# Performance work log

Measured on AMD Instinct MI355X. Metric: run time of the kernel, lower is better.

The kernel has to match this reference:

```python
import jax, jax.numpy as jnp
import numpy as np

B, IN_DIM, EXP_DIM, E = 16384, 256, 128, 8  # batch, input_dim, expert_dim, expert_num


def setup_inputs() -> dict:
    key = jax.random.key(0)
    ks = jax.random.split(key, 12)
    s_in = 1.0 / np.sqrt(IN_DIM)
    return {
        "x_a": jax.random.normal(ks[0], (B, IN_DIM), jnp.float32),
        "x_b": jax.random.normal(ks[1], (B, IN_DIM), jnp.float32),
        "x_share": jax.random.normal(ks[2], (B, IN_DIM), jnp.float32),
        # expert banks: [E, IN_DIM, EXP_DIM] weights, [E, EXP_DIM] bias
        "Wa": jax.random.uniform(ks[3], (E, IN_DIM, EXP_DIM), jnp.float32, -s_in, s_in),
        "ba": jax.random.uniform(ks[4], (E, EXP_DIM), jnp.float32, -s_in, s_in),
        "Wb": jax.random.uniform(ks[5], (E, IN_DIM, EXP_DIM), jnp.float32, -s_in, s_in),
        "bb": jax.random.uniform(ks[6], (E, EXP_DIM), jnp.float32, -s_in, s_in),
        "Ws": jax.random.uniform(ks[7], (E, IN_DIM, EXP_DIM), jnp.float32, -s_in, s_in),
        "bs": jax.random.uniform(ks[8], (E, EXP_DIM), jnp.float32, -s_in, s_in),
        # gate projections (bias=False): num single-output linears == one [num, IN_DIM] matrix
        "Ga": jax.random.uniform(ks[9], (2 * E, IN_DIM), jnp.float32, -s_in, s_in),
        "Gb": jax.random.uniform(ks[10], (2 * E, IN_DIM), jnp.float32, -s_in, s_in),
        "Gs": jax.random.uniform(ks[11], (3 * E, IN_DIM), jnp.float32, -s_in, s_in),
    }


def _experts(x, W, b):
    # batched dense stack: [B,IN] x [E,IN,D] -> [B,E,D]
    return jnp.einsum("bi,eid->bed", x, W) + b[None, :, :]


def _gate(x, G, experts):
    # logits [B, num]; softmax over experts; weighted sum over expert axis
    w = jax.nn.softmax(x @ G.T, axis=1)
    return jnp.einsum("be,bed->bd", w, experts)


def reference(x_a, x_b, x_share, Wa, ba, Wb, bb, Ws, bs, Ga, Gb, Gs):
    ea = _experts(x_a, Wa, ba)          # [B,E,D]
    eb = _experts(x_b, Wb, bb)          # [B,E,D]
    es = _experts(x_share, Ws, bs)      # [B,E,D]
    out_a = _gate(x_a, Ga, jnp.concatenate([ea, es], axis=1))
    out_b = _gate(x_b, Gb, jnp.concatenate([eb, es], axis=1))
    out_s = _gate(x_share, Gs, jnp.concatenate([ea, eb, es], axis=1))
    return (out_a, out_b, out_s)
```

## Files before the change

### kernel.cpp

```cpp
#include <hip/hip_runtime.h>
#include <stdint.h>

#define BATCH 16384
#define INDIM 256
#define DDIM  128
#define NEXP  8
#define ROWS  32

typedef __bf16 bfv8  __attribute__((ext_vector_type(8)));
typedef float  f32x4 __attribute__((ext_vector_type(4)));

__global__ void prep_kernel(const float* __restrict__ Wa, const float* __restrict__ Wb,
                            const float* __restrict__ Ws, const float* __restrict__ Ga,
                            const float* __restrict__ Gb, const float* __restrict__ Gs,
                            __bf16* __restrict__ wp, __bf16* __restrict__ gp) {
    int t = blockIdx.x * 256 + threadIdx.x;
    const int NW = 3 * 8 * 8 * 8 * 64;
    if (t < NW) {
        int lane = t & 63, nt = (t >> 6) & 7, kt = (t >> 9) & 7, e = (t >> 12) & 7, st = t >> 15;
        const float* W = (st == 0) ? Wa : (st == 1) ? Wb : Ws;
        int d  = nt * 16 + (lane & 15);
        int i0 = kt * 32 + (lane >> 4) * 8;
        __bf16* o = wp + (size_t)t * 8;
#pragma unroll
        for (int j = 0; j < 8; j++)
            o[j] = (__bf16)W[(size_t)(e * 256 + i0 + j) * 128 + d];
    } else if (t < NW + 2048) {
        int t2 = t - NW;
        int lane = t2 & 63, nt = (t2 >> 6) & 3, kt = t2 >> 8;
        int g  = nt * 16 + (lane & 15);
        int k0 = kt * 32 + (lane >> 4) * 8;
        __bf16* o = gp + (size_t)t2 * 8;
#pragma unroll
        for (int j = 0; j < 8; j++) {
            int k = k0 + j;
            float v = 0.f;
            if (g < 16)      v = Ga[g * 256 + k];
            else if (g < 32) v = Gb[(g - 16) * 256 + k];
            else if (g < 56) v = Gs[(g - 32) * 256 + k];
            o[j] = (__bf16)v;
        }
    }
}

__device__ __forceinline__ void load_afr(const float* __restrict__ x, int r0,
                                         int l16, int quad, bfv8 afr[2][8]) {
#pragma unroll
    for (int mt = 0; mt < 2; mt++) {
        const float* xr = x + (size_t)(r0 + mt * 16 + l16) * INDIM;
#pragma unroll
        for (int kt = 0; kt < 8; kt++) {
            f32x4 lo = *(const f32x4*)(xr + kt * 32 + quad * 8);
            f32x4 hi = *(const f32x4*)(xr + kt * 32 + quad * 8 + 4);
            bfv8 a;
            a[0] = (__bf16)lo[0]; a[1] = (__bf16)lo[1]; a[2] = (__bf16)lo[2]; a[3] = (__bf16)lo[3];
            a[4] = (__bf16)hi[0]; a[5] = (__bf16)hi[1]; a[6] = (__bf16)hi[2]; a[7] = (__bf16)hi[3];
            afr[mt][kt] = a;
        }
    }
}

__launch_bounds__(256, 2)
__global__ void ple_kernel(const float* __restrict__ xa, const float* __restrict__ xb,
                           const float* __restrict__ xs,
                           const float* __restrict__ ba, const float* __restrict__ bb,
                           const float* __restrict__ bs,
                           const __bf16* __restrict__ wp, const __bf16* __restrict__ gp,
                           float* __restrict__ out) {
    __shared__ float lgt[ROWS * 64];
    __shared__ float wT[64 * ROWS];

    const int tid  = threadIdx.x;
    const int w    = tid >> 6;
    const int lane = tid & 63;
    const int quad = lane >> 4;
    const int l16  = lane & 15;
    const int r0   = blockIdx.x * ROWS;

    bfv8 afr[2][8];

    {
        const float* x = (w == 0) ? xa : (w == 1) ? xb : xs;
        load_afr(x, r0, l16, quad, afr);
        f32x4 acc[2];
#pragma unroll
        for (int mt = 0; mt < 2; mt++) { f32x4 z = {0.f, 0.f, 0.f, 0.f}; acc[mt] = z; }
#pragma unroll
        for (int kt = 0; kt < 8; kt++) {
            bfv8 g = *(const bfv8*)(gp + ((size_t)(kt * 4 + w) * 64 + lane) * 8);
#pragma unroll
            for (int mt = 0; mt < 2; mt++)
                acc[mt] = __builtin_amdgcn_mfma_f32_16x16x32_bf16(afr[mt][kt], g, acc[mt], 0, 0, 0);
        }
#pragma unroll
        for (int mt = 0; mt < 2; mt++)
#pragma unroll
            for (int r = 0; r < 4; r++)
                lgt[(mt * 16 + quad * 4 + r) * 64 + w * 16 + l16] = acc[mt][r];
    }
    __syncthreads();

    if (tid < ROWS) {
        const float* L = lgt + tid * 64;
#pragma unroll
        for (int gi = 0; gi < 3; gi++) {
            const int base = (gi == 0) ? 0 : (gi == 1 ? 16 : 32);
            const int cnt  = (gi == 2) ? 24 : 16;
            float m = -1e30f;
            for (int k = 0; k < cnt; k++) m = fmaxf(m, L[base + k]);
            float s = 0.f;
            for (int k = 0; k < cnt; k++) s += __expf(L[base + k] - m);
            float inv = 1.f / s;
            for (int k = 0; k < cnt; k++) wT[(base + k) * ROWS + tid] = __expf(L[base + k] - m) * inv;
        }
    }
    __syncthreads();

    float o[3][2][2][4];
#pragma unroll
    for (int oi = 0; oi < 3; oi++)
#pragma unroll
        for (int mt = 0; mt < 2; mt++)
#pragma unroll
            for (int ntl = 0; ntl < 2; ntl++)
#pragma unroll
                for (int r = 0; r < 4; r++) o[oi][mt][ntl][r] = 0.f;

#define FOLD(oi, gbase)                                                            \
    {                                                                              \
        _Pragma("unroll")                                                          \
        for (int mt = 0; mt < 2; mt++) {                                           \
            f32x4 wv = *(const f32x4*)(wT + (gbase + eb) * ROWS + mt * 16 + quad * 4); \
            _Pragma("unroll")                                                      \
            for (int ntl = 0; ntl < 2; ntl++)                                      \
                _Pragma("unroll")                                                  \
                for (int r = 0; r < 4; r++)                                        \
                    o[oi][mt][ntl][r] += wv[r] * acc[mt][ntl][r];                  \
        }                                                                          \
    }

    const __bf16* colb = wp + (size_t)(2 * w) * 512 + (size_t)lane * 8;

    bfv8 cb[4][2];
#pragma unroll
    for (int i = 0; i < 4; i++) {
        cb[i][0] = *(const bfv8*)(colb + (size_t)i * 4096);
        cb[i][1] = *(const bfv8*)(colb + (size_t)i * 4096 + 512);
    }

#pragma unroll
    for (int st = 0; st < 3; st++) {
        const float* x    = (st == 0) ? xa : (st == 1) ? xb : xs;
        const float* bias = (st == 0) ? ba : (st == 1) ? bb : bs;
        load_afr(x, r0, l16, quad, afr);

#pragma unroll 1
        for (int eb = 0; eb < NEXP; eb++) {
            float b0 = bias[eb * 128 + w * 32 + l16];
            float b1 = bias[eb * 128 + w * 32 + 16 + l16];

            f32x4 acc[2][2];
#pragma unroll
            for (int mt = 0; mt < 2; mt++)
#pragma unroll
                for (int ntl = 0; ntl < 2; ntl++) { f32x4 z = {0.f, 0.f, 0.f, 0.f}; acc[mt][ntl] = z; }

#pragma unroll
            for (int kt = 0; kt < 8; kt++) {
                const int sl = kt & 3;
                acc[0][0] = __builtin_amdgcn_mfma_f32_16x16x32_bf16(afr[0][kt], cb[sl][0], acc[0][0], 0, 0, 0);
                acc[1][0] = __builtin_amdgcn_mfma_f32_16x16x32_bf16(afr[1][kt], cb[sl][0], acc[1][0], 0, 0, 0);
                acc[0][1] = __builtin_amdgcn_mfma_f32_16x16x32_bf16(afr[0][kt], cb[sl][1], acc[0][1], 0, 0, 0);
                acc[1][1] = __builtin_amdgcn_mfma_f32_16x16x32_bf16(afr[1][kt], cb[sl][1], acc[1][1], 0, 0, 0);
                if (kt < 4 || st < 2 || eb < NEXP - 1) {
                    size_t gpf = (size_t)(st * 64 + eb * 8 + kt + 4) * 4096;
                    cb[sl][0] = *(const bfv8*)(colb + gpf);
                    cb[sl][1] = *(const bfv8*)(colb + gpf + 512);
                }
            }

#pragma unroll
            for (int mt = 0; mt < 2; mt++)
#pragma unroll
                for (int r = 0; r < 4; r++) { acc[mt][0][r] += b0; acc[mt][1][r] += b1; }

            if (st == 0)      { FOLD(0, 0);  FOLD(2, 32); }
            else if (st == 1) { FOLD(1, 16); FOLD(2, 40); }
            else              { FOLD(0, 8);  FOLD(1, 24); FOLD(2, 48); }
        }
    }
#undef FOLD

#pragma unroll
    for (int oi = 0; oi < 3; oi++) {
        float* ob = out + (size_t)oi * BATCH * DDIM;
#pragma unroll
        for (int mt = 0; mt < 2; mt++)
#pragma unroll
            for (int r = 0; r < 4; r++) {
                int row = r0 + mt * 16 + quad * 4 + r;
#pragma unroll
                for (int ntl = 0; ntl < 2; ntl++)
                    ob[(size_t)row * DDIM + w * 32 + ntl * 16 + l16] = o[oi][mt][ntl][r];
            }
    }
}

extern "C" void kernel_launch(void* const* d_in, const int* in_sizes, int n_in,
                              void* d_out, int out_size, void* d_ws, size_t ws_size,
                              hipStream_t stream) {
    const float* xa = (const float*)d_in[0];
    const float* xb = (const float*)d_in[1];
    const float* xs = (const float*)d_in[2];
    const float* Wa = (const float*)d_in[3];
    const float* ba = (const float*)d_in[4];
    const float* Wb = (const float*)d_in[5];
    const float* bb = (const float*)d_in[6];
    const float* Ws = (const float*)d_in[7];
    const float* bs = (const float*)d_in[8];
    const float* Ga = (const float*)d_in[9];
    const float* Gb = (const float*)d_in[10];
    const float* Gs = (const float*)d_in[11];

    __bf16* wp = (__bf16*)d_ws;
    __bf16* gp = wp + 3 * 8 * 8 * 8 * 64 * 8;

    prep_kernel<<<392, 256, 0, stream>>>(Wa, Wb, Ws, Ga, Gb, Gs, wp, gp);
    ple_kernel<<<BATCH / ROWS, 256, 0, stream>>>(xa, xb, xs, ba, bb, bs, wp, gp, (float*)d_out);
}
```

Measured before the change: 166.6 us.

## Use 512-thread blocks with shared bf16 activations and warp-parallel softmax

Blocks grow to 8 waves, each owning 16 output columns instead of 32. The three input tiles are converted to bf16 once, cooperatively, and staged in shared memory instead of each wave loading and converting them into registers. The gate softmax now runs inside the MFMA waves using shuffle reductions, replacing the serial 32-thread loop. This aims to cut redundant global loads and register pressure so occupancy rises, at the cost of more shared-memory reads in the inner loop and extra barriers.

```diff
diff --git a/kernel.cpp b/kernel.cpp
--- a/kernel.cpp
+++ b/kernel.cpp
@@ -43,32 +43,16 @@
     }
 }
 
-__device__ __forceinline__ void load_afr(const float* __restrict__ x, int r0,
-                                         int l16, int quad, bfv8 afr[2][8]) {
-#pragma unroll
-    for (int mt = 0; mt < 2; mt++) {
-        const float* xr = x + (size_t)(r0 + mt * 16 + l16) * INDIM;
-#pragma unroll
-        for (int kt = 0; kt < 8; kt++) {
-            f32x4 lo = *(const f32x4*)(xr + kt * 32 + quad * 8);
-            f32x4 hi = *(const f32x4*)(xr + kt * 32 + quad * 8 + 4);
-            bfv8 a;
-            a[0] = (__bf16)lo[0]; a[1] = (__bf16)lo[1]; a[2] = (__bf16)lo[2]; a[3] = (__bf16)lo[3];
-            a[4] = (__bf16)hi[0]; a[5] = (__bf16)hi[1]; a[6] = (__bf16)hi[2]; a[7] = (__bf16)hi[3];
-            afr[mt][kt] = a;
-        }
-    }
-}
-
-__launch_bounds__(256, 2)
+__launch_bounds__(512, 4)
 __global__ void ple_kernel(const float* __restrict__ xa, const float* __restrict__ xb,
                            const float* __restrict__ xs,
                            const float* __restrict__ ba, const float* __restrict__ bb,
                            const float* __restrict__ bs,
                            const __bf16* __restrict__ wp, const __bf16* __restrict__ gp,
                            float* __restrict__ out) {
-    __shared__ float lgt[ROWS * 64];
-    __shared__ float wT[64 * ROWS];
+    __shared__ __bf16 xlds[3 * 16 * 512];
+    __shared__ float  wT[64 * ROWS];
+    __shared__ float  pm[2][ROWS], ps[2][ROWS], cm[ROWS], civ[ROWS];
 
     const int tid  = threadIdx.x;
     const int w    = tid >> 6;
@@ -77,112 +61,157 @@
     const int l16  = lane & 15;
     const int r0   = blockIdx.x * ROWS;
 
-    bfv8 afr[2][8];
-
-    {
-        const float* x = (w == 0) ? xa : (w == 1) ? xb : xs;
-        load_afr(x, r0, l16, quad, afr);
-        f32x4 acc[2];
-#pragma unroll
-        for (int mt = 0; mt < 2; mt++) { f32x4 z = {0.f, 0.f, 0.f, 0.f}; acc[mt] = z; }
+    const __bf16* colb = wp + (size_t)w * 512 + (size_t)lane * 8;
+    bfv8 cb[8];
+#pragma unroll
+    for (int i = 0; i < 8; i++)
+        cb[i] = *(const bfv8*)(colb + (size_t)i * 4096);
+
+#pragma unroll
+    for (int i = 0; i < 6; i++) {
+        int gidx = w * 6 + i;
+        int st = gidx >> 4, rem = gidx & 15, mt = rem >> 3, kt = rem & 7;
+        const float* x = (st == 0) ? xa : (st == 1) ? xb : xs;
+        const float* xr = x + (size_t)(r0 + mt * 16 + l16) * INDIM + kt * 32 + quad * 8;
+        f32x4 lo = *(const f32x4*)xr;
+        f32x4 hi = *(const f32x4*)(xr + 4);
+        bfv8 a;
+        a[0] = (__bf16)lo[0]; a[1] = (__bf16)lo[1]; a[2] = (__bf16)lo[2]; a[3] = (__bf16)lo[3];
+        a[4] = (__bf16)hi[0]; a[5] = (__bf16)hi[1]; a[6] = (__bf16)hi[2]; a[7] = (__bf16)hi[3];
+        *(bfv8*)&xlds[(size_t)(st * 16 + mt * 8 + kt) * 512 + lane * 8] = a;
+    }
+    __syncthreads();
+
+    float e_[2][4], mx_[2][4];
+    if (w < 4) {
+        const int gst = (w < 2) ? w : 2;
+        f32x4 acc0 = {0.f, 0.f, 0.f, 0.f}, acc1 = {0.f, 0.f, 0.f, 0.f};
 #pragma unroll
         for (int kt = 0; kt < 8; kt++) {
-            bfv8 g = *(const bfv8*)(gp + ((size_t)(kt * 4 + w) * 64 + lane) * 8);
-#pragma unroll
-            for (int mt = 0; mt < 2; mt++)
-                acc[mt] = __builtin_amdgcn_mfma_f32_16x16x32_bf16(afr[mt][kt], g, acc[mt], 0, 0, 0);
-        }
-#pragma unroll
-        for (int mt = 0; mt < 2; mt++)
+            bfv8 g  = *(const bfv8*)(gp + ((size_t)(kt * 4 + w) * 64 + lane) * 8);
+            bfv8 a0 = *(const bfv8*)&xlds[(size_t)(gst * 16 + kt) * 512 + lane * 8];
+            bfv8 a1 = *(const bfv8*)&xlds[(size_t)(gst * 16 + 8 + kt) * 512 + lane * 8];
+            acc0 = __builtin_amdgcn_mfma_f32_16x16x32_bf16(a0, g, acc0, 0, 0, 0);
+            acc1 = __builtin_amdgcn_mfma_f32_16x16x32_bf16(a1, g, acc1, 0, 0, 0);
+        }
+        float la[2][4];
+#pragma unroll
+        for (int r = 0; r < 4; r++) { la[0][r] = acc0[r]; la[1][r] = acc1[r]; }
+        if (w == 3 && l16 >= 8) {
+#pragma unroll
+            for (int mt = 0; mt < 2; mt++)
+#pragma unroll
+                for (int r = 0; r < 4; r++) la[mt][r] = -1e30f;
+        }
+        float mx[2][4];
+#pragma unroll
+        for (int mt = 0; mt < 2; mt++)
+#pragma unroll
+            for (int r = 0; r < 4; r++) mx[mt][r] = la[mt][r];
+#pragma unroll
+        for (int m = 1; m <= 8; m <<= 1)
+#pragma unroll
+            for (int mt = 0; mt < 2; mt++)
+#pragma unroll
+                for (int r = 0; r < 4; r++)
+                    mx[mt][r] = fmaxf(mx[mt][r], __shfl_xor(mx[mt][r], m));
+        float ex[2][4], sm[2][4];
+#pragma unroll
+        for (int mt = 0; mt < 2; mt++)
+#pragma unroll
+            for (int r = 0; r < 4; r++) { ex[mt][r] = __expf(la[mt][r] - mx[mt][r]); sm[mt][r] = ex[mt][r]; }
+#pragma unroll
+        for (int m = 1; m <= 8; m <<= 1)
+#pragma unroll
+            for (int mt = 0; mt < 2; mt++)
+#pragma unroll
+                for (int r = 0; r < 4; r++)
+                    sm[mt][r] += __shfl_xor(sm[mt][r], m);
+        if (w < 2) {
+#pragma unroll
+            for (int mt = 0; mt < 2; mt++)
+#pragma unroll
+                for (int r = 0; r < 4; r++)
+                    wT[(w * 16 + l16) * ROWS + mt * 16 + quad * 4 + r] = ex[mt][r] / sm[mt][r];
+        } else {
+#pragma unroll
+            for (int mt = 0; mt < 2; mt++)
+#pragma unroll
+                for (int r = 0; r < 4; r++) { e_[mt][r] = ex[mt][r]; mx_[mt][r] = mx[mt][r]; }
+            if (l16 == 0) {
+#pragma unroll
+                for (int mt = 0; mt < 2; mt++)
+#pragma unroll
+                    for (int r = 0; r < 4; r++) {
+                        pm[w - 2][mt * 16 + quad * 4 + r] = mx[mt][r];
+                        ps[w - 2][mt * 16 + quad * 4 + r] = sm[mt][r];
+                    }
+            }
+        }
+    }
+    __syncthreads();
+    if (tid < ROWS) {
+        float m0 = pm[0][tid], m1 = pm[1][tid];
+        float M = fmaxf(m0, m1);
+        float S = ps[0][tid] * __expf(m0 - M) + ps[1][tid] * __expf(m1 - M);
+        cm[tid] = M; civ[tid] = 1.f / S;
+    }
+    __syncthreads();
+    if (w == 2 || w == 3) {
+        const int base = (w == 2) ? 32 : 48;
+#pragma unroll
+        for (int mt = 0; mt < 2; mt++) {
+            f32x4 cmv = *(const f32x4*)&cm[mt * 16 + quad * 4];
+            f32x4 cvv = *(const f32x4*)&civ[mt * 16 + quad * 4];
 #pragma unroll
             for (int r = 0; r < 4; r++)
-                lgt[(mt * 16 + quad * 4 + r) * 64 + w * 16 + l16] = acc[mt][r];
-    }
-    __syncthreads();
-
-    if (tid < ROWS) {
-        const float* L = lgt + tid * 64;
-#pragma unroll
-        for (int gi = 0; gi < 3; gi++) {
-            const int base = (gi == 0) ? 0 : (gi == 1 ? 16 : 32);
-            const int cnt  = (gi == 2) ? 24 : 16;
-            float m = -1e30f;
-            for (int k = 0; k < cnt; k++) m = fmaxf(m, L[base + k]);
-            float s = 0.f;
-            for (int k = 0; k < cnt; k++) s += __expf(L[base + k] - m);
-            float inv = 1.f / s;
-            for (int k = 0; k < cnt; k++) wT[(base + k) * ROWS + tid] = __expf(L[base + k] - m) * inv;
-        }
-    }
-    __syncthreads();
-
-    float o[3][2][2][4];
+                wT[(base + l16) * ROWS + mt * 16 + quad * 4 + r] =
+                    e_[mt][r] * __expf(mx_[mt][r] - cmv[r]) * cvv[r];
+        }
+    }
+    __syncthreads();
+
+    float o[3][2][4];
 #pragma unroll
     for (int oi = 0; oi < 3; oi++)
 #pragma unroll
         for (int mt = 0; mt < 2; mt++)
 #pragma unroll
-            for (int ntl = 0; ntl < 2; ntl++)
-#pragma unroll
-                for (int r = 0; r < 4; r++) o[oi][mt][ntl][r] = 0.f;
-
-#define FOLD(oi, gbase)                                                            \
-    {                                                                              \
-        _Pragma("unroll")                                                          \
-        for (int mt = 0; mt < 2; mt++) {                                           \
-            f32x4 wv = *(const f32x4*)(wT + (gbase + eb) * ROWS + mt * 16 + quad * 4); \
-            _Pragma("unroll")                                                      \
-            for (int ntl = 0; ntl < 2; ntl++)                                      \
-                _Pragma("unroll")                                                  \
-                for (int r = 0; r < 4; r++)                                        \
-                    o[oi][mt][ntl][r] += wv[r] * acc[mt][ntl][r];                  \
-        }                                                                          \
-    }
-
-    const __bf16* colb = wp + (size_t)(2 * w) * 512 + (size_t)lane * 8;
-
-    bfv8 cb[4][2];
-#pragma unroll
-    for (int i = 0; i < 4; i++) {
-        cb[i][0] = *(const bfv8*)(colb + (size_t)i * 4096);
-        cb[i][1] = *(const bfv8*)(colb + (size_t)i * 4096 + 512);
+            for (int r = 0; r < 4; r++) o[oi][mt][r] = 0.f;
+
+#define FOLD(oi, gbase)                                                       \
+    {                                                                         \
+        f32x4 wv0 = *(const f32x4*)&wT[(gbase + eb) * ROWS + quad * 4];       \
+        f32x4 wv1 = *(const f32x4*)&wT[(gbase + eb) * ROWS + 16 + quad * 4];  \
+        _Pragma("unroll")                                                     \
+        for (int r = 0; r < 4; r++) {                                         \
+            o[oi][0][r] += wv0[r] * acc0[r];                                  \
+            o[oi][1][r] += wv1[r] * acc1[r];                                  \
+        }                                                                     \
     }
 
 #pragma unroll
     for (int st = 0; st < 3; st++) {
-        const float* x    = (st == 0) ? xa : (st == 1) ? xb : xs;
         const float* bias = (st == 0) ? ba : (st == 1) ? bb : bs;
-        load_afr(x, r0, l16, quad, afr);
+        const __bf16* aB = &xlds[(size_t)(st * 16) * 512 + lane * 8];
 
 #pragma unroll 1
         for (int eb = 0; eb < NEXP; eb++) {
-            float b0 = bias[eb * 128 + w * 32 + l16];
-            float b1 = bias[eb * 128 + w * 32 + 16 + l16];
-
-            f32x4 acc[2][2];
-#pragma unroll
-            for (int mt = 0; mt < 2; mt++)
-#pragma unroll
-                for (int ntl = 0; ntl < 2; ntl++) { f32x4 z = {0.f, 0.f, 0.f, 0.f}; acc[mt][ntl] = z; }
-
+            float b0 = bias[eb * 128 + w * 16 + l16];
+
+            f32x4 acc0 = {0.f, 0.f, 0.f, 0.f}, acc1 = {0.f, 0.f, 0.f, 0.f};
 #pragma unroll
             for (int kt = 0; kt < 8; kt++) {
-                const int sl = kt & 3;
-                acc[0][0] = __builtin_amdgcn_mfma_f32_16x16x32_bf16(afr[0][kt], cb[sl][0], acc[0][0], 0, 0, 0);
-                acc[1][0] = __builtin_amdgcn_mfma_f32_16x16x32_bf16(afr[1][kt], cb[sl][0], acc[1][0], 0, 0, 0);
-                acc[0][1] = __builtin_amdgcn_mfma_f32_16x16x32_bf16(afr[0][kt], cb[sl][1], acc[0][1], 0, 0, 0);
-                acc[1][1] = __builtin_amdgcn_mfma_f32_16x16x32_bf16(afr[1][kt], cb[sl][1], acc[1][1], 0, 0, 0);
-                if (kt < 4 || st < 2 || eb < NEXP - 1) {
-                    size_t gpf = (size_t)(st * 64 + eb * 8 + kt + 4) * 4096;
-                    cb[sl][0] = *(const bfv8*)(colb + gpf);
-                    cb[sl][1] = *(const bfv8*)(colb + gpf + 512);
-                }
+                bfv8 a0 = *(const bfv8*)(aB + (size_t)kt * 512);
+                bfv8 a1 = *(const bfv8*)(aB + (size_t)(8 + kt) * 512);
+                acc0 = __builtin_amdgcn_mfma_f32_16x16x32_bf16(a0, cb[kt], acc0, 0, 0, 0);
+                acc1 = __builtin_amdgcn_mfma_f32_16x16x32_bf16(a1, cb[kt], acc1, 0, 0, 0);
+                if (st < 2 || eb < NEXP - 1)
+                    cb[kt] = *(const bfv8*)(colb + (size_t)(st * 64 + eb * 8 + kt + 8) * 4096);
             }
 
 #pragma unroll
-            for (int mt = 0; mt < 2; mt++)
-#pragma unroll
-                for (int r = 0; r < 4; r++) { acc[mt][0][r] += b0; acc[mt][1][r] += b1; }
+            for (int r = 0; r < 4; r++) { acc0[r] += b0; acc1[r] += b0; }
 
             if (st == 0)      { FOLD(0, 0);  FOLD(2, 32); }
             else if (st == 1) { FOLD(1, 16); FOLD(2, 40); }
@@ -199,9 +228,7 @@
 #pragma unroll
             for (int r = 0; r < 4; r++) {
                 int row = r0 + mt * 16 + quad * 4 + r;
-#pragma unroll
-                for (int ntl = 0; ntl < 2; ntl++)
-                    ob[(size_t)row * DDIM + w * 32 + ntl * 16 + l16] = o[oi][mt][ntl][r];
+                ob[(size_t)row * DDIM + w * 16 + l16] = o[oi][mt][r];
             }
     }
 }
@@ -226,5 +253,5 @@
     __bf16* gp = wp + 3 * 8 * 8 * 8 * 64 * 8;
 
     prep_kernel<<<392, 256, 0, stream>>>(Wa, Wb, Ws, Ga, Gb, Gs, wp, gp);
-    ple_kernel<<<BATCH / ROWS, 256, 0, stream>>>(xa, xb, xs, ba, bb, bs, wp, gp, (float*)d_out);
+    ple_kernel<<<BATCH / ROWS, 512, 0, stream>>>(xa, xb, xs, ba, bb, bs, wp, gp, (float*)d_out);
 }
```

Result: slower. 175.9 us (+5.6%).
